# Performance work log

Hardware: AMD Instinct MI355X
Metric: run time of the kernel (lower is better)

Reference implementation:

```python
import jax, jax.numpy as jnp
import numpy as np

T, N, F_IN, H, E, OUT = 24, 20000, 64, 256, 320000, 1


def setup_inputs() -> dict:
    key = jax.random.key(0)
    ks = jax.random.split(key, 16)
    inp = {
        "x": jax.random.normal(ks[0], (T, N, F_IN), dtype=jnp.float32),
        "edge_index": jax.random.randint(ks[1], (2, E), 0, N, dtype=jnp.int32),
        "edge_weight": jax.random.uniform(ks[2], (E,), dtype=jnp.float32),
        # GCNConv 1 (input_size -> hidden)
        "W1": jax.random.normal(ks[3], (F_IN, H), dtype=jnp.float32) / np.sqrt(F_IN),
        "b1": jnp.zeros((H,), dtype=jnp.float32),
        # GCNConv 2 (hidden -> hidden)
        "W2": jax.random.normal(ks[4], (H, H), dtype=jnp.float32) / np.sqrt(H),
        "b2": jnp.zeros((H,), dtype=jnp.float32),
        # LayerNorm affine
        "ln_w": jnp.ones((H,), dtype=jnp.float32),
        "ln_b": jnp.zeros((H,), dtype=jnp.float32),
        # GRU (1 layer): weight_ih [3H,H_in], weight_hh [3H,H]
        "Wih": jax.random.normal(ks[5], (3 * H, H), dtype=jnp.float32) / np.sqrt(H),
        "Whh": jax.random.normal(ks[6], (3 * H, H), dtype=jnp.float32) / np.sqrt(H),
        "bih": jnp.zeros((3 * H,), dtype=jnp.float32),
        "bhh": jnp.zeros((3 * H,), dtype=jnp.float32),
        # fc
        "Wfc": jax.random.normal(ks[7], (OUT, H), dtype=jnp.float32) / np.sqrt(H),
        "bfc": jnp.zeros((OUT,), dtype=jnp.float32),
    }
    return inp


def _gcn_norm(edge_index, edge_weight, n_nodes):
    # PyG gcn_norm with self-loops (fill=1.0) and symmetric normalization.
    loop = jnp.arange(n_nodes, dtype=edge_index.dtype)
    src = jnp.concatenate([edge_index[0], loop])
    dst = jnp.concatenate([edge_index[1], loop])
    ew = jnp.concatenate([edge_weight, jnp.ones((n_nodes,), edge_weight.dtype)])
    deg = jax.ops.segment_sum(ew, dst, num_segments=n_nodes)
    dinv = jnp.where(deg > 0, jax.lax.rsqrt(deg), 0.0)
    norm = dinv[src] * ew * dinv[dst]
    return src, dst, norm


def _gcn_conv(x, src, dst, norm, W, b, n_nodes):
    h = x @ W                              # [N, out]
    msg = norm[:, None] * h[src]           # [E+N, out]
    out = jax.ops.segment_sum(msg, dst, num_segments=n_nodes)
    return out + b


def reference(x, edge_index, edge_weight, W1, b1, W2, b2, ln_w, ln_b,
              Wih, Whh, bih, bhh, Wfc, bfc):
    n_nodes = x.shape[1]
    src, dst, norm = _gcn_norm(edge_index, edge_weight, n_nodes)

    def encode(xt):  # xt: [N, F_IN]
        h = _gcn_conv(xt, src, dst, norm, W1, b1, n_nodes)
        h = jnp.where(h >= 0, h, 0.01 * h)  # leaky_relu, slope 0.01
        h = _gcn_conv(h, src, dst, norm, W2, b2, n_nodes)
        mu = jnp.mean(h, axis=-1, keepdims=True)
        var = jnp.mean(jnp.square(h - mu), axis=-1, keepdims=True)
        return (h - mu) * jax.lax.rsqrt(var + 1e-5) * ln_w + ln_b

    seq = jax.vmap(encode)(x)  # [T, N, H]

    def gru_step(h, xt):
        gi = xt @ Wih.T + bih
        gh = h @ Whh.T + bhh
        ir, iz, inn = jnp.split(gi, 3, axis=-1)
        hr, hz, hn = jnp.split(gh, 3, axis=-1)
        r = jax.nn.sigmoid(ir + hr)
        z = jax.nn.sigmoid(iz + hz)
        n = jnp.tanh(inn + r * hn)
        h_new = (1.0 - z) * n + z * h
        return h_new, None

    h0 = jnp.zeros((n_nodes, Whh.shape[1]), dtype=x.dtype)
    h_last, _ = jax.lax.scan(gru_step, h0, seq)
    return h_last @ Wfc.T + bfc  # [N, OUT]
```

## Files before the change

kernel.cpp:

```cpp
#include <hip/hip_runtime.h>
#include <math.h>

#define T_STEPS 24
#define N_NODES 20000
#define F_IN 64
#define H_DIM 256
#define H3 (3 * H_DIM)
#define TC 4
#define NCHUNK (T_STEPS / TC)
#define GRU_BM_GRPS 160

using f16x8 = __attribute__((ext_vector_type(8))) _Float16;
using f16x4 = __attribute__((ext_vector_type(4))) _Float16;
using f16x2 = __attribute__((ext_vector_type(2))) _Float16;
using f32x4 = __attribute__((ext_vector_type(4))) float;

__device__ __forceinline__ void gload_lds16(const void* g, void* l) {
    __builtin_amdgcn_global_load_lds(
        (const __attribute__((address_space(1))) void*)(uintptr_t)g,
        (__attribute__((address_space(3))) void*)l, 16, 0, 0);
}

__device__ __forceinline__ float sigmoidf_(float x) { return 1.0f / (1.0f + expf(-x)); }

__global__ void init_deg_kernel(float* deg, int* indeg, int n) {
    int i = blockIdx.x * blockDim.x + threadIdx.x;
    if (i < n) { deg[i] = 1.0f; indeg[i] = 0; }
}

__global__ void accum_deg_kernel(const int* __restrict__ src, const int* __restrict__ dst,
                                 const float* __restrict__ ew, float* deg, int* indeg, int E) {
    int e = blockIdx.x * blockDim.x + threadIdx.x;
    if (e < E) {
        atomicAdd(&deg[dst[e]], ew[e]);
        atomicAdd(&indeg[dst[e]], 1);
    }
}

__global__ void dinv_kernel(float* deg, float* selfnorm, int n) {
    int i = blockIdx.x * blockDim.x + threadIdx.x;
    if (i < n) {
        float d = deg[i];
        float di = (d > 0.0f) ? rsqrtf(d) : 0.0f;
        deg[i] = di;
        selfnorm[i] = di * di;
    }
}

__global__ void edge_norm_kernel(const int* __restrict__ src, const int* __restrict__ dst,
                                 const float* __restrict__ ew, const float* __restrict__ dinv,
                                 float* norm, int E) {
    int e = blockIdx.x * blockDim.x + threadIdx.x;
    if (e < E) norm[e] = dinv[src[e]] * ew[e] * dinv[dst[e]];
}

__global__ void scan_kernel(const int* __restrict__ indeg, int* offs, int* cursor, int N) {
    __shared__ int part[1024];
    int t = threadIdx.x;
    const int CH = (N + 1023) / 1024;
    int s = 0;
    for (int i = 0; i < CH; i++) {
        int idx = t * CH + i;
        if (idx < N) s += indeg[idx];
    }
    part[t] = s;
    __syncthreads();
    for (int off = 1; off < 1024; off <<= 1) {
        int v = (t >= off) ? part[t - off] : 0;
        __syncthreads();
        part[t] += v;
        __syncthreads();
    }
    int base = (t == 0) ? 0 : part[t - 1];
    for (int i = 0; i < CH; i++) {
        int idx = t * CH + i;
        if (idx < N) {
            offs[idx] = base;
            cursor[idx] = base;
            base += indeg[idx];
        }
    }
    if (t == 0) offs[N] = part[1023];
}

__global__ void csr_fill_kernel(const int* __restrict__ src, const int* __restrict__ dst,
                                const float* __restrict__ norm, int* cursor,
                                int* csr_src, float* csr_norm, int E) {
    int e = blockIdx.x * blockDim.x + threadIdx.x;
    if (e < E) {
        int d = dst[e];
        int pos = atomicAdd(&cursor[d], 1);
        csr_src[pos] = src[e];
        csr_norm[pos] = norm[e];
    }
}

__global__ void pack_b16_kernel(const float* __restrict__ W, _Float16* __restrict__ P,
                                int K, int Nn, int trans) {
    int idx = blockIdx.x * blockDim.x + threadIdx.x;
    int total = (K >> 3) * Nn;
    if (idx >= total) return;
    int kk = idx / Nn, c = idx - kk * Nn;
    int n = c;
    if (trans == 2) {
        int a = c / 48, w = c % 48;
        int g = w >> 4, b = w & 15;
        n = g * 256 + a * 16 + b;
    }
    size_t o = (size_t)idx * 8;
    for (int j = 0; j < 8; ++j) {
        float v = (trans != 0) ? W[(size_t)n * K + kk * 8 + j] : W[(size_t)(kk * 8 + j) * Nn + n];
        P[o + j] = (_Float16)v;
    }
}

__global__ void perm_bias_kernel(const float* __restrict__ b, float* __restrict__ pb) {
    int c = blockIdx.x * blockDim.x + threadIdx.x;
    if (c < H3) {
        int a = c / 48, w = c % 48;
        int g = w >> 4, bb = w & 15;
        pb[c] = b[g * 256 + a * 16 + bb];
    }
}

__global__ void tofp16_kernel(const float* __restrict__ in, _Float16* __restrict__ out, int n4) {
    int i = blockIdx.x * blockDim.x + threadIdx.x;
    if (i < n4) {
        float4 v = ((const float4*)in)[i];
        f16x4 o = { (_Float16)v.x, (_Float16)v.y, (_Float16)v.z, (_Float16)v.w };
        ((f16x4*)out)[i] = o;
    }
}

__global__ void agg1_kernel(const _Float16* __restrict__ xs, const int* __restrict__ offs,
                            const int* __restrict__ csr_src, const float* __restrict__ csr_norm,
                            const float* __restrict__ selfnorm,
                            _Float16* __restrict__ out, int N) {
    int t = blockIdx.y;
    int n = blockIdx.x * 4 + (threadIdx.x >> 6);
    int lane = threadIdx.x & 63;
    int fg = lane & 7, ep = lane >> 3;
    const _Float16* xsl = xs + (size_t)t * N * F_IN;
    float acc[8] = {};
    int e0 = offs[n], e1 = offs[n + 1];
    int e = e0 + ep;
    for (; e + 8 < e1; e += 16) {
        int sA = csr_src[e], sB = csr_src[e + 8];
        float wA = csr_norm[e], wB = csr_norm[e + 8];
        f16x8 vA = *(const f16x8*)&xsl[(size_t)sA * F_IN + fg * 8];
        f16x8 vB = *(const f16x8*)&xsl[(size_t)sB * F_IN + fg * 8];
#pragma unroll
        for (int c = 0; c < 8; ++c) acc[c] = fmaf(wA, (float)vA[c], acc[c]);
#pragma unroll
        for (int c = 0; c < 8; ++c) acc[c] = fmaf(wB, (float)vB[c], acc[c]);
    }
    if (e < e1) {
        int s = csr_src[e];
        float w = csr_norm[e];
        f16x8 v = *(const f16x8*)&xsl[(size_t)s * F_IN + fg * 8];
#pragma unroll
        for (int c = 0; c < 8; ++c) acc[c] = fmaf(w, (float)v[c], acc[c]);
    }
#pragma unroll
    for (int c = 0; c < 8; ++c) {
        acc[c] += __shfl_xor(acc[c], 8, 64);
        acc[c] += __shfl_xor(acc[c], 16, 64);
        acc[c] += __shfl_xor(acc[c], 32, 64);
    }
    f16x8 own = *(const f16x8*)&xsl[(size_t)n * F_IN + fg * 8];
    float sn = selfnorm[n];
#pragma unroll
    for (int c = 0; c < 8; ++c) acc[c] = fmaf(sn, (float)own[c], acc[c]);
    if (ep == 0) {
        f16x8 o;
#pragma unroll
        for (int c = 0; c < 8; ++c) o[c] = (_Float16)acc[c];
        *(f16x8*)&out[((size_t)t * N + n) * F_IN + fg * 8] = o;
    }
}

__global__ void agg2_kernel(const _Float16* __restrict__ hs, const int* __restrict__ offs,
                            const int* __restrict__ csr_src, const float* __restrict__ csr_norm,
                            const float* __restrict__ selfnorm,
                            _Float16* __restrict__ out, int N) {
    int t = blockIdx.y;
    int n = blockIdx.x * 4 + (threadIdx.x >> 6);
    int lane = threadIdx.x & 63;
    int half = lane >> 5, fl = lane & 31;
    const _Float16* hsl = hs + (size_t)t * N * H_DIM;
    float acc[8] = {};
    int e0 = offs[n], e1 = offs[n + 1];
    int e = e0 + half;
    for (; e + 2 < e1; e += 4) {
        int sA = csr_src[e], sB = csr_src[e + 2];
        float wA = csr_norm[e], wB = csr_norm[e + 2];
        f16x8 vA = *(const f16x8*)&hsl[(size_t)sA * H_DIM + fl * 8];
        f16x8 vB = *(const f16x8*)&hsl[(size_t)sB * H_DIM + fl * 8];
#pragma unroll
        for (int c = 0; c < 8; ++c) acc[c] = fmaf(wA, (float)vA[c], acc[c]);
#pragma unroll
        for (int c = 0; c < 8; ++c) acc[c] = fmaf(wB, (float)vB[c], acc[c]);
    }
    if (e < e1) {
        int s = csr_src[e];
        float w = csr_norm[e];
        f16x8 v = *(const f16x8*)&hsl[(size_t)s * H_DIM + fl * 8];
#pragma unroll
        for (int c = 0; c < 8; ++c) acc[c] = fmaf(w, (float)v[c], acc[c]);
    }
#pragma unroll
    for (int c = 0; c < 8; ++c) acc[c] += __shfl_xor(acc[c], 32, 64);
    f16x8 own = *(const f16x8*)&hsl[(size_t)n * H_DIM + fl * 8];
    float sn = selfnorm[n];
#pragma unroll
    for (int c = 0; c < 8; ++c) acc[c] = fmaf(sn, (float)own[c], acc[c]);
    if (half == 0) {
        f16x8 o;
#pragma unroll
        for (int c = 0; c < 8; ++c) o[c] = (_Float16)acc[c];
        *(f16x8*)&out[((size_t)t * N + n) * H_DIM + fl * 8] = o;
    }
}

__global__ __launch_bounds__(256, 4)
void conv1_kernel(const _Float16* __restrict__ A, const _Float16* __restrict__ Bp,
                  const float* __restrict__ bias, _Float16* __restrict__ C16,
                  int M, int Nn, int K) {
    __shared__ _Float16 As[4][128][8];
    __shared__ _Float16 Bs[4][128][8];

    const int tid = threadIdx.x;
    const int wave = tid >> 6, lane = tid & 63;
    const int bm = blockIdx.x * 128, bn = blockIdx.y * 128;
    const int wm = (wave >> 1) * 64, wn = (wave & 1) * 64;
    const int kq = lane >> 4, r = lane & 15;

    f32x4 acc[4][4];
#pragma unroll
    for (int i = 0; i < 4; ++i)
#pragma unroll
        for (int j = 0; j < 4; ++j) acc[i][j] = (f32x4){0.f, 0.f, 0.f, 0.f};

    for (int k0 = 0; k0 < K; k0 += 32) {
        __syncthreads();
        const int kb = k0 >> 3;
#pragma unroll
        for (int it = 0; it < 2; ++it) {
            int c = it * 256 + tid;
            int kk = c >> 7, idx = c & 127;
            int row = bm + idx;
            if (row >= M) row = M - 1;
            size_t aoff = (size_t)row * K + k0 + kk * 8;
            size_t boff = ((size_t)(kb + kk) * Nn + bn + idx) * 8;
            gload_lds16(A + aoff, &As[0][0][0] + (size_t)c * 8);
            gload_lds16(Bp + boff, &Bs[0][0][0] + (size_t)c * 8);
        }
        __syncthreads();

        f16x8 a[4], b[4];
#pragma unroll
        for (int f = 0; f < 4; ++f) {
            a[f] = *(const f16x8*)&As[kq][wm + f * 16 + r][0];
            b[f] = *(const f16x8*)&Bs[kq][wn + f * 16 + r][0];
        }
#pragma unroll
        for (int i = 0; i < 4; ++i)
#pragma unroll
            for (int j = 0; j < 4; ++j)
                acc[i][j] = __builtin_amdgcn_mfma_f32_16x16x32_f16(a[i], b[j], acc[i][j], 0, 0, 0);
    }

#pragma unroll
    for (int j = 0; j < 4; ++j) {
        int col = bn + wn + j * 16 + r;
        float bv = bias[col];
#pragma unroll
        for (int i = 0; i < 4; ++i) {
#pragma unroll
            for (int q = 0; q < 4; ++q) {
                int row = bm + wm + i * 16 + kq * 4 + q;
                if (row < M) {
                    float v = acc[i][j][q] + bv;
                    v = (v >= 0.0f) ? v : 0.01f * v;
                    C16[(size_t)row * Nn + col] = (_Float16)v;
                }
            }
        }
    }
}

__global__ __launch_bounds__(256, 2)
void conv2ln_kernel(const _Float16* __restrict__ A, const _Float16* __restrict__ Bp,
                    const float* __restrict__ b2, const float* __restrict__ lnw,
                    const float* __restrict__ lnb, _Float16* __restrict__ out, int M) {
    __shared__ _Float16 As[4][128][8];
    __shared__ _Float16 Bs[4][256][8];
    __shared__ float lnP[128][2][2];

    const int tid = threadIdx.x;
    const int wave = tid >> 6, lane = tid & 63;
    const int bm = blockIdx.x * 128;
    const int wm = (wave >> 1) * 64, wn = (wave & 1) * 128;
    const int cw = wave & 1;
    const int kq = lane >> 4, r = lane & 15;

    f32x4 acc[4][8];
#pragma unroll
    for (int i = 0; i < 4; ++i)
#pragma unroll
        for (int j = 0; j < 8; ++j) acc[i][j] = (f32x4){0.f, 0.f, 0.f, 0.f};

    for (int k0 = 0; k0 < H_DIM; k0 += 32) {
        __syncthreads();
        const int kb = k0 >> 3;
#pragma unroll
        for (int it = 0; it < 2; ++it) {
            int c = it * 256 + tid;
            int kk = c >> 7, idx = c & 127;
            int row = bm + idx;
            if (row >= M) row = M - 1;
            gload_lds16(A + (size_t)row * H_DIM + k0 + kk * 8, &As[0][0][0] + (size_t)c * 8);
        }
#pragma unroll
        for (int it = 0; it < 4; ++it) {
            int c = it * 256 + tid;
            int kk = c >> 8, col = c & 255;
            gload_lds16(Bp + ((size_t)(kb + kk) * H_DIM + col) * 8, &Bs[0][0][0] + (size_t)c * 8);
        }
        __syncthreads();

        f16x8 a[4], b[8];
#pragma unroll
        for (int f = 0; f < 4; ++f) a[f] = *(const f16x8*)&As[kq][wm + f * 16 + r][0];
#pragma unroll
        for (int f = 0; f < 8; ++f) b[f] = *(const f16x8*)&Bs[kq][wn + f * 16 + r][0];
#pragma unroll
        for (int i = 0; i < 4; ++i)
#pragma unroll
            for (int j = 0; j < 8; ++j)
                acc[i][j] = __builtin_amdgcn_mfma_f32_16x16x32_f16(a[i], b[j], acc[i][j], 0, 0, 0);
    }

#pragma unroll
    for (int i = 0; i < 4; ++i) {
#pragma unroll
        for (int q = 0; q < 4; ++q) {
            float s = 0.f, s2 = 0.f;
#pragma unroll
            for (int j = 0; j < 8; ++j) {
                float v = acc[i][j][q] + b2[wn + j * 16 + r];
                acc[i][j][q] = v;
                s += v;
                s2 += v * v;
            }
#pragma unroll
            for (int m = 1; m < 16; m <<= 1) {
                s += __shfl_xor(s, m, 64);
                s2 += __shfl_xor(s2, m, 64);
            }
            int lrow = wm + i * 16 + kq * 4 + q;
            if (r == 0) { lnP[lrow][cw][0] = s; lnP[lrow][cw][1] = s2; }
        }
    }
    __syncthreads();

#pragma unroll
    for (int i = 0; i < 4; ++i) {
#pragma unroll
        for (int q = 0; q < 4; ++q) {
            int lrow = wm + i * 16 + kq * 4 + q;
            int row = bm + lrow;
            float S = lnP[lrow][0][0] + lnP[lrow][1][0];
            float S2 = lnP[lrow][0][1] + lnP[lrow][1][1];
            float mu = S * (1.0f / H_DIM);
            float var = S2 * (1.0f / H_DIM) - mu * mu;
            float rstd = rsqrtf(var + 1e-5f);
            if (row < M) {
#pragma unroll
                for (int j = 0; j < 8; ++j) {
                    int col = wn + j * 16 + r;
                    float o = (acc[i][j][q] - mu) * rstd * lnw[col] + lnb[col];
                    out[(size_t)row * H_DIM + col] = (_Float16)o;
                }
            }
        }
    }
}

__global__ __launch_bounds__(256, 3)
void gru_step_kernel(const _Float16* __restrict__ hprev, const _Float16* __restrict__ e,
                     const _Float16* __restrict__ Bhh, const _Float16* __restrict__ Bih,
                     const float* __restrict__ pbhh, const float* __restrict__ pbih,
                     _Float16* __restrict__ hnew, int M) {
    const int bid = blockIdx.x;
    const int bn_grp = bid / GRU_BM_GRPS;
    const int bm_grp = bid - bn_grp * GRU_BM_GRPS;
    if (bm_grp * 128 >= M) return;
    const int bm = bm_grp * 128, bn = bn_grp * 96;

    __shared__ _Float16 Ah[4][128][8];
    __shared__ _Float16 Ae[4][128][8];
    __shared__ _Float16 Bsh[4][96][8];
    __shared__ _Float16 Bsi[4][96][8];

    const int tid = threadIdx.x;
    const int wave = tid >> 6, lane = tid & 63;
    const int wm = (wave >> 1) * 64, wn = (wave & 1) * 48;
    const int kq = lane >> 4, r = lane & 15;

    f32x4 arz[4][2], ahn[4], ainn[4];
#pragma unroll
    for (int i = 0; i < 4; ++i) {
        arz[i][0] = (f32x4){0.f, 0.f, 0.f, 0.f};
        arz[i][1] = (f32x4){0.f, 0.f, 0.f, 0.f};
        ahn[i] = (f32x4){0.f, 0.f, 0.f, 0.f};
        ainn[i] = (f32x4){0.f, 0.f, 0.f, 0.f};
    }

    for (int k0 = 0; k0 < H_DIM; k0 += 32) {
        __syncthreads();
        const int kb = k0 >> 3;
#pragma unroll
        for (int it = 0; it < 2; ++it) {
            int c = it * 256 + tid;
            int kk = c >> 7, idx = c & 127;
            int row = bm + idx;
            if (row >= M) row = M - 1;
            size_t ao = (size_t)row * H_DIM + k0 + kk * 8;
            gload_lds16(hprev + ao, &Ah[0][0][0] + (size_t)c * 8);
            gload_lds16(e + ao, &Ae[0][0][0] + (size_t)c * 8);
        }
        {
            int c = tid;
            int kk = c / 96, col = c - kk * 96;
            size_t bo = ((size_t)(kb + kk) * H3 + bn + col) * 8;
            gload_lds16(Bhh + bo, &Bsh[0][0][0] + (size_t)c * 8);
            gload_lds16(Bih + bo, &Bsi[0][0][0] + (size_t)c * 8);
            if (tid < 128) {
                int c2 = 256 + tid;
                int kk2 = c2 / 96, col2 = c2 - kk2 * 96;
                size_t bo2 = ((size_t)(kb + kk2) * H3 + bn + col2) * 8;
                gload_lds16(Bhh + bo2, &Bsh[0][0][0] + (size_t)c2 * 8);
                gload_lds16(Bih + bo2, &Bsi[0][0][0] + (size_t)c2 * 8);
            }
        }
        __syncthreads();

        f16x8 ah[4], ae[4], bh[3], bi[3];
#pragma unroll
        for (int f = 0; f < 4; ++f) {
            ah[f] = *(const f16x8*)&Ah[kq][wm + f * 16 + r][0];
            ae[f] = *(const f16x8*)&Ae[kq][wm + f * 16 + r][0];
        }
#pragma unroll
        for (int f = 0; f < 3; ++f) {
            bh[f] = *(const f16x8*)&Bsh[kq][wn + f * 16 + r][0];
            bi[f] = *(const f16x8*)&Bsi[kq][wn + f * 16 + r][0];
        }
#pragma unroll
        for (int i = 0; i < 4; ++i) {
            arz[i][0] = __builtin_amdgcn_mfma_f32_16x16x32_f16(ah[i], bh[0], arz[i][0], 0, 0, 0);
            arz[i][0] = __builtin_amdgcn_mfma_f32_16x16x32_f16(ae[i], bi[0], arz[i][0], 0, 0, 0);
            arz[i][1] = __builtin_amdgcn_mfma_f32_16x16x32_f16(ah[i], bh[1], arz[i][1], 0, 0, 0);
            arz[i][1] = __builtin_amdgcn_mfma_f32_16x16x32_f16(ae[i], bi[1], arz[i][1], 0, 0, 0);
            ahn[i] = __builtin_amdgcn_mfma_f32_16x16x32_f16(ah[i], bh[2], ahn[i], 0, 0, 0);
            ainn[i] = __builtin_amdgcn_mfma_f32_16x16x32_f16(ae[i], bi[2], ainn[i], 0, 0, 0);
        }
    }

    const int colbase = bn + wn;
    const int agrp = colbase / 48;
    const int f = agrp * 16 + r;
    const float b_r = pbhh[colbase + r] + pbih[colbase + r];
    const float b_z = pbhh[colbase + 16 + r] + pbih[colbase + 16 + r];
    const float b_hn = pbhh[colbase + 32 + r];
    const float b_in = pbih[colbase + 32 + r];
#pragma unroll
    for (int i = 0; i < 4; ++i) {
#pragma unroll
        for (int q = 0; q < 4; ++q) {
            int row = bm + wm + i * 16 + kq * 4 + q;
            if (row < M) {
                float rg = sigmoidf_(arz[i][0][q] + b_r);
                float zg = sigmoidf_(arz[i][1][q] + b_z);
                float nn = tanhf(ainn[i][q] + b_in + rg * (ahn[i][q] + b_hn));
                float hp = (float)hprev[(size_t)row * H_DIM + f];
                hnew[(size_t)row * H_DIM + f] = (_Float16)((1.0f - zg) * nn + zg * hp);
            }
        }
    }
}

__global__ void fc_kernel(const _Float16* __restrict__ h, const float* __restrict__ Wfc,
                          const float* __restrict__ bfc, float* __restrict__ out, int N) {
    int n = blockIdx.x * 4 + (threadIdx.x >> 6);
    int lane = threadIdx.x & 63;
    if (n >= N) return;
    f16x4 hv = *(const f16x4*)&h[(size_t)n * H_DIM + lane * 4];
    float4 wv = *(const float4*)&Wfc[lane * 4];
    float acc = (float)hv[0] * wv.x + (float)hv[1] * wv.y + (float)hv[2] * wv.z + (float)hv[3] * wv.w;
#pragma unroll
    for (int o = 32; o > 0; o >>= 1) acc += __shfl_down(acc, o, 64);
    if (lane == 0) out[n] = acc + bfc[0];
}

extern "C" void kernel_launch(void* const* d_in, const int* in_sizes, int n_in,
                              void* d_out, int out_size, void* d_ws, size_t ws_size,
                              hipStream_t stream) {
    const float* x   = (const float*)d_in[0];
    const int* eidx  = (const int*)d_in[1];
    const float* ew  = (const float*)d_in[2];
    const float* W1  = (const float*)d_in[3];
    const float* b1  = (const float*)d_in[4];
    const float* W2  = (const float*)d_in[5];
    const float* b2  = (const float*)d_in[6];
    const float* lnw = (const float*)d_in[7];
    const float* lnb = (const float*)d_in[8];
    const float* Wih = (const float*)d_in[9];
    const float* Whh = (const float*)d_in[10];
    const float* bih = (const float*)d_in[11];
    const float* bhh = (const float*)d_in[12];
    const float* Wfc = (const float*)d_in[13];
    const float* bfc = (const float*)d_in[14];

    const int E = in_sizes[2];
    const int N = N_NODES;
    const int* src = eidx;
    const int* dst = eidx + E;

    uintptr_t p = (uintptr_t)d_ws;
    auto alloc = [&](size_t bytes) -> void* {
        p = (p + 255) & ~(uintptr_t)255;
        void* r = (void*)p;
        p += bytes;
        return r;
    };
    float* deg      = (float*)alloc(N * sizeof(float));
    float* selfnorm = (float*)alloc(N * sizeof(float));
    float* norm     = (float*)alloc(E * sizeof(float));
    int* indeg      = (int*)alloc(N * sizeof(int));
    int* offs       = (int*)alloc((N + 1) * sizeof(int));
    int* cursor     = (int*)alloc(N * sizeof(int));
    int* csr_src    = (int*)alloc(E * sizeof(int));
    float* csr_norm = (float*)alloc(E * sizeof(float));
    _Float16* W1p   = (_Float16*)alloc((size_t)F_IN * H_DIM * sizeof(_Float16));
    _Float16* W2p   = (_Float16*)alloc((size_t)H_DIM * H_DIM * sizeof(_Float16));
    _Float16* Wihp  = (_Float16*)alloc((size_t)H_DIM * H3 * sizeof(_Float16));
    _Float16* Whhp  = (_Float16*)alloc((size_t)H_DIM * H3 * sizeof(_Float16));
    float* pbih     = (float*)alloc(H3 * sizeof(float));
    float* pbhh     = (float*)alloc(H3 * sizeof(float));
    _Float16* xs16  = (_Float16*)alloc((size_t)TC * N * F_IN * sizeof(_Float16));
    _Float16* a1_16 = (_Float16*)alloc((size_t)TC * N * F_IN * sizeof(_Float16));
    _Float16* h1_16 = (_Float16*)alloc((size_t)TC * N * H_DIM * sizeof(_Float16));
    _Float16* a2_16 = (_Float16*)alloc((size_t)TC * N * H_DIM * sizeof(_Float16));
    _Float16* e16   = (_Float16*)alloc((size_t)TC * N * H_DIM * sizeof(_Float16));
    _Float16* h_a   = (_Float16*)alloc((size_t)N * H_DIM * sizeof(_Float16));
    _Float16* h_b   = (_Float16*)alloc((size_t)N * H_DIM * sizeof(_Float16));

    const int TB = 256;
    hipLaunchKernelGGL(init_deg_kernel, dim3((N + TB - 1) / TB), dim3(TB), 0, stream, deg, indeg, N);
    hipLaunchKernelGGL(accum_deg_kernel, dim3((E + TB - 1) / TB), dim3(TB), 0, stream, src, dst, ew, deg, indeg, E);
    hipLaunchKernelGGL(dinv_kernel, dim3((N + TB - 1) / TB), dim3(TB), 0, stream, deg, selfnorm, N);
    hipLaunchKernelGGL(edge_norm_kernel, dim3((E + TB - 1) / TB), dim3(TB), 0, stream, src, dst, ew, deg, norm, E);
    hipLaunchKernelGGL(scan_kernel, dim3(1), dim3(1024), 0, stream, indeg, offs, cursor, N);
    hipLaunchKernelGGL(csr_fill_kernel, dim3((E + TB - 1) / TB), dim3(TB), 0, stream, src, dst, norm, cursor, csr_src, csr_norm, E);

    {
        int tot = (F_IN / 8) * H_DIM;
        hipLaunchKernelGGL(pack_b16_kernel, dim3((tot + TB - 1) / TB), dim3(TB), 0, stream, W1, W1p, F_IN, H_DIM, 0);
        tot = (H_DIM / 8) * H_DIM;
        hipLaunchKernelGGL(pack_b16_kernel, dim3((tot + TB - 1) / TB), dim3(TB), 0, stream, W2, W2p, H_DIM, H_DIM, 0);
        tot = (H_DIM / 8) * H3;
        hipLaunchKernelGGL(pack_b16_kernel, dim3((tot + TB - 1) / TB), dim3(TB), 0, stream, Wih, Wihp, H_DIM, H3, 2);
        hipLaunchKernelGGL(pack_b16_kernel, dim3((tot + TB - 1) / TB), dim3(TB), 0, stream, Whh, Whhp, H_DIM, H3, 2);
        hipLaunchKernelGGL(perm_bias_kernel, dim3((H3 + TB - 1) / TB), dim3(TB), 0, stream, bih, pbih);
        hipLaunchKernelGGL(perm_bias_kernel, dim3((H3 + TB - 1) / TB), dim3(TB), 0, stream, bhh, pbhh);
    }

    hipMemsetAsync(h_a, 0, (size_t)N * H_DIM * sizeof(_Float16), stream);

    const int MC = TC * N;
    dim3 gb(256);
    dim3 g_conv1(MC / 128, H_DIM / 128);
    dim3 g_c2ln(MC / 128);
    dim3 g_gru(8 * GRU_BM_GRPS);
    dim3 g_agg(N / 4, TC);

    _Float16* h_cur = h_a;
    _Float16* h_nxt = h_b;

    for (int chunk = 0; chunk < NCHUNK; ++chunk) {
        const float* xc = x + (size_t)chunk * TC * N * F_IN;
        int n4 = TC * N * F_IN / 4;
        hipLaunchKernelGGL(tofp16_kernel, dim3((n4 + TB - 1) / TB), dim3(TB), 0, stream, xc, xs16, n4);
        hipLaunchKernelGGL(agg1_kernel, g_agg, dim3(256), 0, stream,
                           xs16, offs, csr_src, csr_norm, selfnorm, a1_16, N);
        hipLaunchKernelGGL(conv1_kernel, g_conv1, gb, 0, stream,
                           a1_16, W1p, b1, h1_16, MC, H_DIM, F_IN);
        hipLaunchKernelGGL(agg2_kernel, g_agg, dim3(256), 0, stream,
                           h1_16, offs, csr_src, csr_norm, selfnorm, a2_16, N);
        hipLaunchKernelGGL(conv2ln_kernel, g_c2ln, gb, 0, stream,
                           a2_16, W2p, b2, lnw, lnb, e16, MC);
        for (int tc = 0; tc < TC; ++tc) {
            hipLaunchKernelGGL(gru_step_kernel, g_gru, gb, 0, stream,
                               h_cur, e16 + (size_t)tc * N * H_DIM, Whhp, Wihp,
                               pbhh, pbih, h_nxt, N);
            _Float16* tmp = h_cur; h_cur = h_nxt; h_nxt = tmp;
        }
    }

    hipLaunchKernelGGL(fc_kernel, dim3((N + 3) / 4), dim3(256), 0, stream, h_cur, Wfc, bfc, (float*)d_out, N);
}
```

Measured before the change: 2.351 ms.

## Transpose MFMA operands for vectorized epilogue stores and widen agg2 edge unroll

In the conv1, conv2+LayerNorm and GRU kernels the MFMA A/B operands are swapped, so each lane's accumulator holds four consecutive columns of one row instead of four rows of one column. The epilogues then use float4 bias/weight loads and 8-byte f16x4 stores, and the LayerNorm row reduction needs only two cross-lane shuffles instead of four per row. Separately, the agg2 gather loop is unrolled to process four edges per half-wave per iteration, giving more outstanding loads. The conv1 epilogue drops its row<M bound check, which could write out of bounds if M is not a multiple of the tile.

After: 2.176 ms. 1.08x faster.

```diff
diff --git a/kernel.cpp b/kernel.cpp
--- a/kernel.cpp
+++ b/kernel.cpp
@@ -190,18 +190,33 @@
     const _Float16* hsl = hs + (size_t)t * N * H_DIM;
     float acc[8] = {};
     int e0 = offs[n], e1 = offs[n + 1];
-    int e = e0 + half;
-    for (; e + 2 < e1; e += 4) {
-        int sA = csr_src[e], sB = csr_src[e + 2];
-        float wA = csr_norm[e], wB = csr_norm[e + 2];
-        f16x8 vA = *(const f16x8*)&hsl[(size_t)sA * H_DIM + fl * 8];
-        f16x8 vB = *(const f16x8*)&hsl[(size_t)sB * H_DIM + fl * 8];
-#pragma unroll
-        for (int c = 0; c < 8; ++c) acc[c] = fmaf(wA, (float)vA[c], acc[c]);
-#pragma unroll
-        for (int c = 0; c < 8; ++c) acc[c] = fmaf(wB, (float)vB[c], acc[c]);
-    }
-    if (e < e1) {
+    int e = e0;
+    for (; e + 8 <= e1; e += 8) {
+        int eb = e + half * 4;
+        int s0 = csr_src[eb], s1 = csr_src[eb + 1], s2 = csr_src[eb + 2], s3 = csr_src[eb + 3];
+        float w0 = csr_norm[eb], w1 = csr_norm[eb + 1], w2 = csr_norm[eb + 2], w3 = csr_norm[eb + 3];
+        f16x8 v0 = *(const f16x8*)&hsl[(size_t)s0 * H_DIM + fl * 8];
+        f16x8 v1 = *(const f16x8*)&hsl[(size_t)s1 * H_DIM + fl * 8];
+        f16x8 v2 = *(const f16x8*)&hsl[(size_t)s2 * H_DIM + fl * 8];
+        f16x8 v3 = *(const f16x8*)&hsl[(size_t)s3 * H_DIM + fl * 8];
+#pragma unroll
+        for (int c = 0; c < 8; ++c) acc[c] = fmaf(w0, (float)v0[c], acc[c]);
+#pragma unroll
+        for (int c = 0; c < 8; ++c) acc[c] = fmaf(w1, (float)v1[c], acc[c]);
+#pragma unroll
+        for (int c = 0; c < 8; ++c) acc[c] = fmaf(w2, (float)v2[c], acc[c]);
+#pragma unroll
+        for (int c = 0; c < 8; ++c) acc[c] = fmaf(w3, (float)v3[c], acc[c]);
+    }
+    for (; e + 2 <= e1; e += 2) {
+        int eb = e + half;
+        int s = csr_src[eb];
+        float w = csr_norm[eb];
+        f16x8 v = *(const f16x8*)&hsl[(size_t)s * H_DIM + fl * 8];
+#pragma unroll
+        for (int c = 0; c < 8; ++c) acc[c] = fmaf(w, (float)v[c], acc[c]);
+    }
+    if (e < e1 && half == 0) {
         int s = csr_src[e];
         float w = csr_norm[e];
         f16x8 v = *(const f16x8*)&hsl[(size_t)s * H_DIM + fl * 8];
@@ -267,24 +282,24 @@
         for (int i = 0; i < 4; ++i)
 #pragma unroll
             for (int j = 0; j < 4; ++j)
-                acc[i][j] = __builtin_amdgcn_mfma_f32_16x16x32_f16(a[i], b[j], acc[i][j], 0, 0, 0);
+                acc[i][j] = __builtin_amdgcn_mfma_f32_16x16x32_f16(b[j], a[i], acc[i][j], 0, 0, 0);
     }
 
 #pragma unroll
     for (int j = 0; j < 4; ++j) {
-        int col = bn + wn + j * 16 + r;
-        float bv = bias[col];
+        int colb = bn + wn + j * 16 + kq * 4;
+        float4 bv = *(const float4*)&bias[colb];
 #pragma unroll
         for (int i = 0; i < 4; ++i) {
+            int row = bm + wm + i * 16 + r;
+            f16x4 o;
 #pragma unroll
             for (int q = 0; q < 4; ++q) {
-                int row = bm + wm + i * 16 + kq * 4 + q;
-                if (row < M) {
-                    float v = acc[i][j][q] + bv;
-                    v = (v >= 0.0f) ? v : 0.01f * v;
-                    C16[(size_t)row * Nn + col] = (_Float16)v;
-                }
+                float v = acc[i][j][q] + ((const float*)&bv)[q];
+                v = (v >= 0.0f) ? v : 0.01f * v;
+                o[q] = (_Float16)v;
             }
+            *(f16x4*)&C16[(size_t)row * Nn + colb] = o;
         }
     }
 }
@@ -338,51 +353,49 @@
         for (int i = 0; i < 4; ++i)
 #pragma unroll
             for (int j = 0; j < 8; ++j)
-                acc[i][j] = __builtin_amdgcn_mfma_f32_16x16x32_f16(a[i], b[j], acc[i][j], 0, 0, 0);
+                acc[i][j] = __builtin_amdgcn_mfma_f32_16x16x32_f16(b[j], a[i], acc[i][j], 0, 0, 0);
     }
 
 #pragma unroll
     for (int i = 0; i < 4; ++i) {
-#pragma unroll
-        for (int q = 0; q < 4; ++q) {
-            float s = 0.f, s2 = 0.f;
-#pragma unroll
-            for (int j = 0; j < 8; ++j) {
-                float v = acc[i][j][q] + b2[wn + j * 16 + r];
+        float s = 0.f, s2 = 0.f;
+#pragma unroll
+        for (int j = 0; j < 8; ++j) {
+            float4 bv = *(const float4*)&b2[wn + j * 16 + kq * 4];
+#pragma unroll
+            for (int q = 0; q < 4; ++q) {
+                float v = acc[i][j][q] + ((const float*)&bv)[q];
                 acc[i][j][q] = v;
                 s += v;
                 s2 += v * v;
             }
-#pragma unroll
-            for (int m = 1; m < 16; m <<= 1) {
-                s += __shfl_xor(s, m, 64);
-                s2 += __shfl_xor(s2, m, 64);
-            }
-            int lrow = wm + i * 16 + kq * 4 + q;
-            if (r == 0) { lnP[lrow][cw][0] = s; lnP[lrow][cw][1] = s2; }
-        }
+        }
+        s += __shfl_xor(s, 16, 64);  s2 += __shfl_xor(s2, 16, 64);
+        s += __shfl_xor(s, 32, 64);  s2 += __shfl_xor(s2, 32, 64);
+        int lrow = wm + i * 16 + r;
+        if (kq == 0) { lnP[lrow][cw][0] = s; lnP[lrow][cw][1] = s2; }
     }
     __syncthreads();
 
 #pragma unroll
     for (int i = 0; i < 4; ++i) {
-#pragma unroll
-        for (int q = 0; q < 4; ++q) {
-            int lrow = wm + i * 16 + kq * 4 + q;
-            int row = bm + lrow;
-            float S = lnP[lrow][0][0] + lnP[lrow][1][0];
-            float S2 = lnP[lrow][0][1] + lnP[lrow][1][1];
-            float mu = S * (1.0f / H_DIM);
-            float var = S2 * (1.0f / H_DIM) - mu * mu;
-            float rstd = rsqrtf(var + 1e-5f);
-            if (row < M) {
-#pragma unroll
-                for (int j = 0; j < 8; ++j) {
-                    int col = wn + j * 16 + r;
-                    float o = (acc[i][j][q] - mu) * rstd * lnw[col] + lnb[col];
-                    out[(size_t)row * H_DIM + col] = (_Float16)o;
-                }
-            }
+        int lrow = wm + i * 16 + r;
+        int row = bm + lrow;
+        float S = lnP[lrow][0][0] + lnP[lrow][1][0];
+        float S2 = lnP[lrow][0][1] + lnP[lrow][1][1];
+        float mu = S * (1.0f / H_DIM);
+        float var = S2 * (1.0f / H_DIM) - mu * mu;
+        float rstd = rsqrtf(var + 1e-5f);
+#pragma unroll
+        for (int j = 0; j < 8; ++j) {
+            int colb = wn + j * 16 + kq * 4;
+            float4 wv = *(const float4*)&lnw[colb];
+            float4 bvv = *(const float4*)&lnb[colb];
+            f16x4 o;
+#pragma unroll
+            for (int q = 0; q < 4; ++q)
+                o[q] = (_Float16)((acc[i][j][q] - mu) * rstd * ((const float*)&wv)[q] + ((const float*)&bvv)[q]);
+            *(f16x4*)&out[(size_t)row * H_DIM + colb] = o;
         }
     }
 }
@@ -459,34 +472,41 @@
         }
 #pragma unroll
         for (int i = 0; i < 4; ++i) {
-            arz[i][0] = __builtin_amdgcn_mfma_f32_16x16x32_f16(ah[i], bh[0], arz[i][0], 0, 0, 0);
-            arz[i][0] = __builtin_amdgcn_mfma_f32_16x16x32_f16(ae[i], bi[0], arz[i][0], 0, 0, 0);
-            arz[i][1] = __builtin_amdgcn_mfma_f32_16x16x32_f16(ah[i], bh[1], arz[i][1], 0, 0, 0);
-            arz[i][1] = __builtin_amdgcn_mfma_f32_16x16x32_f16(ae[i], bi[1], arz[i][1], 0, 0, 0);
-            ahn[i] = __builtin_amdgcn_mfma_f32_16x16x32_f16(ah[i], bh[2], ahn[i], 0, 0, 0);
-            ainn[i] = __builtin_amdgcn_mfma_f32_16x16x32_f16(ae[i], bi[2], ainn[i], 0, 0, 0);
+            arz[i][0] = __builtin_amdgcn_mfma_f32_16x16x32_f16(bh[0], ah[i], arz[i][0], 0, 0, 0);
+            arz[i][0] = __builtin_amdgcn_mfma_f32_16x16x32_f16(bi[0], ae[i], arz[i][0], 0, 0, 0);
+            arz[i][1] = __builtin_amdgcn_mfma_f32_16x16x32_f16(bh[1], ah[i], arz[i][1], 0, 0, 0);
+            arz[i][1] = __builtin_amdgcn_mfma_f32_16x16x32_f16(bi[1], ae[i], arz[i][1], 0, 0, 0);
+            ahn[i] = __builtin_amdgcn_mfma_f32_16x16x32_f16(bh[2], ah[i], ahn[i], 0, 0, 0);
+            ainn[i] = __builtin_amdgcn_mfma_f32_16x16x32_f16(bi[2], ae[i], ainn[i], 0, 0, 0);
         }
     }
 
     const int colbase = bn + wn;
     const int agrp = colbase / 48;
-    const int f = agrp * 16 + r;
-    const float b_r = pbhh[colbase + r] + pbih[colbase + r];
-    const float b_z = pbhh[colbase + 16 + r] + pbih[colbase + 16 + r];
-    const float b_hn = pbhh[colbase + 32 + r];
-    const float b_in = pbih[colbase + 32 + r];
+    const int fb = agrp * 16 + kq * 4;
+    float b_r[4], b_z[4], b_hn[4], b_in[4];
+#pragma unroll
+    for (int q = 0; q < 4; ++q) {
+        int cq = colbase + kq * 4 + q;
+        b_r[q]  = pbhh[cq] + pbih[cq];
+        b_z[q]  = pbhh[cq + 16] + pbih[cq + 16];
+        b_hn[q] = pbhh[cq + 32];
+        b_in[q] = pbih[cq + 32];
+    }
 #pragma unroll
     for (int i = 0; i < 4; ++i) {
-#pragma unroll
-        for (int q = 0; q < 4; ++q) {
-            int row = bm + wm + i * 16 + kq * 4 + q;
-            if (row < M) {
-                float rg = sigmoidf_(arz[i][0][q] + b_r);
-                float zg = sigmoidf_(arz[i][1][q] + b_z);
-                float nn = tanhf(ainn[i][q] + b_in + rg * (ahn[i][q] + b_hn));
-                float hp = (float)hprev[(size_t)row * H_DIM + f];
-                hnew[(size_t)row * H_DIM + f] = (_Float16)((1.0f - zg) * nn + zg * hp);
+        int row = bm + wm + i * 16 + r;
+        if (row < M) {
+            f16x4 hp = *(const f16x4*)&hprev[(size_t)row * H_DIM + fb];
+            f16x4 o;
+#pragma unroll
+            for (int q = 0; q < 4; ++q) {
+                float rg = sigmoidf_(arz[i][0][q] + b_r[q]);
+                float zg = sigmoidf_(arz[i][1][q] + b_z[q]);
+                float nn = tanhf(ainn[i][q] + b_in[q] + rg * (ahn[i][q] + b_hn[q]));
+                o[q] = (_Float16)((1.0f - zg) * nn + zg * (float)hp[q]);
             }
+            *(f16x4*)&hnew[(size_t)row * H_DIM + fb] = o;
         }
     }
 }
```
